# Optimization experiments

Hardware: AMD Instinct MI355X
Metric: run time of the kernel (lower is better)

## Reference

```python
import jax, jax.numpy as jnp
import numpy as np

D_MODEL = 256
N_FEATURES = 32768
N_BLOCKS = 8
MIN_FEATURES = 512
BATCH = 2048
ALPHA = 0.99          # RunningAvgNormalizer alpha
EPS_CTRL = 3e-4       # L1RegController eps
TARGET_L0 = 100.0


def _pareto_seg(n_features, n_blocks, min_features, rng):
    # mirrors get_pareto_block_bounds, returning per-feature block ids
    cdf = 1.0 - (np.arange(n_features - min_features + 1) / (n_features - min_features + 1)) ** 0.5
    pdf = np.concatenate([np.zeros(min_features), np.abs(cdf[1:] - cdf[:-1])])
    pdf = pdf / pdf.sum()
    sp = np.sort(rng.choice(n_features, size=n_blocks - 1, replace=False, p=pdf))
    return np.searchsorted(sp, np.arange(n_features), side='right').astype(np.int32)


def setup_inputs() -> dict:
    key = jax.random.key(0)
    k0, k1 = jax.random.split(key, 2)
    x = jax.random.normal(k0, (BATCH, D_MODEL), jnp.float32)
    W_enc = jax.random.normal(k1, (D_MODEL, N_FEATURES), jnp.float32) / np.sqrt(D_MODEL)
    b_enc = -0.04 * jnp.ones((N_FEATURES,), jnp.float32)
    W_dec = (0.1 * W_enc / jnp.linalg.norm(W_enc, axis=0, keepdims=True)).T
    b_dec = jnp.zeros((D_MODEL,), jnp.float32)
    bw = np.arange(1, N_BLOCKS + 1, dtype=np.float32) ** 1.0  # block_weight_power = 1.0
    block_weights = jnp.asarray(bw / bw.max())
    running_avg = jnp.asarray([np.sqrt(D_MODEL)], jnp.float32)  # warmed-up running norm
    l1_scale = jnp.ones((1,), jnp.float32)
    seg = jnp.asarray(_pareto_seg(N_FEATURES, N_BLOCKS, MIN_FEATURES, np.random.default_rng(0)))
    return {"x": x, "W_enc": W_enc, "b_enc": b_enc, "W_dec": W_dec, "b_dec": b_dec,
            "block_weights": block_weights, "running_avg": running_avg,
            "l1_scale": l1_scale, "seg": seg}


def reference(x, W_enc, b_enc, W_dec, b_dec, block_weights, running_avg, l1_scale, seg):
    K = block_weights.shape[0]
    B, d = x.shape
    # RunningAvgNormalizer.normalize(update=True): update EMA, then scale (no grad through EMA)
    ra = ALPHA * running_avg[0] + (1.0 - ALPHA) * jnp.mean(jnp.linalg.norm(x, axis=-1))
    ra = jax.lax.stop_gradient(ra)
    xn = x * (jnp.sqrt(jnp.float32(d)) / ra)
    acts = jax.nn.relu(xn @ W_enc + b_enc)                       # [B, F]
    Wd_norms = jnp.linalg.norm(W_dec, axis=1)                    # [F]
    # per-block log-loss: sum over block features of mean-over-batch log term
    per_feat = jnp.mean(jnp.log(acts * Wd_norms + 0.1) - jnp.log(0.1), axis=0)  # [F]
    block_l1 = jax.ops.segment_sum(per_feat, seg, num_segments=K)               # [K]
    l1_loss = jnp.mean(block_weights * jnp.cumsum(block_l1))
    # per-block decode: (acts masked to block) @ W_dec, sequential over K small blocks
    onehot = (seg[None, :] == jnp.arange(K)[:, None]).astype(acts.dtype)  # [K, F]
    block_preds = jax.lax.map(lambda m: (acts * m) @ W_dec, onehot)       # [K, B, d]
    cum_preds = jnp.cumsum(block_preds, axis=0) + b_dec                   # b_dec added to preds[0] pre-cumsum
    block_errs = jnp.mean(jnp.sum((cum_preds - xn[None]) ** 2, axis=-1), axis=-1) * block_weights
    mse_loss = jnp.mean(block_errs)
    # L1RegController (no-grad)
    avg_l0 = jax.lax.stop_gradient(jnp.sum(acts > 0).astype(jnp.float32) / B)
    l1_reg_scale = jnp.where(avg_l0 < TARGET_L0, l1_scale[0] * (1.0 - EPS_CTRL), l1_scale[0] * (1.0 + EPS_CTRL))
    loss = mse_loss + l1_reg_scale * l1_loss
    return loss
```

## Files before the change

### kernel.cpp

```cpp
#include <hip/hip_runtime.h>

typedef float  f32x4  __attribute__((ext_vector_type(4)));
typedef __bf16 bf16x8 __attribute__((ext_vector_type(8)));
typedef __bf16 bf16x4 __attribute__((ext_vector_type(4)));
typedef unsigned short u16;

#define BATCH 2048
#define DM    256
#define NFEAT 32768
#define NBLK  8
#define ALPHA_C   0.99f
#define EPS_CTRL  3e-4f
#define TARGET_L0 100.0f

#define BT    32
#define FC    2048
#define NCHUNK (NFEAT / FC)
#define MACRO 128
#define NMACRO (FC / MACRO)
#define NPMAX 24
#define ACTS_SZ (BT * MACRO)

#define WS_RA    0
#define WS_SCALE 1
#define WS_L0    2
#define WS_L1    4
#define WS_ERR   16
#define WSI_BND  32
#define WSI_PTN  40
#define WSI_PTS  41
#define WSI_PSEG 66
#define WS_WDN   256
#define PIECES_OFF_BYTES ((size_t)262144)
#define PIECES_BYTES ((size_t)NPMAX * BATCH * DM * 2)
#define WEP_OFF_BYTES (PIECES_OFF_BYTES + PIECES_BYTES)
#define WDP_OFF_BYTES (WEP_OFF_BYTES + (size_t)NFEAT * DM * 2)

#define RAW_BARRIER() asm volatile("s_waitcnt lgkmcnt(0)\n\ts_barrier" ::: "memory")

static __device__ inline u16 f2b(float f) {
    return __builtin_bit_cast(u16, (__bf16)f);
}
static __device__ inline float b2f(u16 u) {
    return (float)__builtin_bit_cast(__bf16, u);
}
static __device__ inline f32x4 mfma16(bf16x8 a, bf16x8 b, f32x4 c) {
    return __builtin_amdgcn_mfma_f32_16x16x32_bf16(a, b, c, 0, 0, 0);
}

__global__ __launch_bounds__(256) void k_prep(const float* __restrict__ x,
                                              const int* __restrict__ seg,
                                              float* ws) {
    const int bid = blockIdx.x;
    const int wave = threadIdx.x >> 6, lane = threadIdx.x & 63;
    if (bid < BATCH / 4) {
        const int row = bid * 4 + wave;
        const float4 v = *reinterpret_cast<const float4*>(x + (size_t)row * DM + lane * 4);
        float s = v.x * v.x + v.y * v.y + v.z * v.z + v.w * v.w;
        #pragma unroll
        for (int o = 32; o; o >>= 1) s += __shfl_xor(s, o);
        if (lane == 0) atomicAdd(&ws[WS_RA], sqrtf(s));
    } else {
        const int f = (bid - BATCH / 4) * 256 + threadIdx.x;
        if (f > 0 && f < NFEAT) {
            const int s = seg[f];
            if (s != seg[f - 1]) ((int*)ws)[WSI_BND + s] = f;
        }
    }
}

__global__ void k_pt2(const int* __restrict__ seg,
                      const float* __restrict__ ravg, float* ws) {
    __shared__ int stv[NCHUNK + NBLK];
    __shared__ int outL[NPMAX];
    __shared__ int NL;
    int* wsi = (int*)ws;
    const int t = threadIdx.x;
    if (t < NCHUNK) stv[t] = t * FC;
    else if (t < NCHUNK + NBLK - 1) stv[t] = wsi[WSI_BND + (t - NCHUNK + 1)];
    __syncthreads();
    if (t == 0) {
        int i = 0, j = NCHUNK, N = 0;
        while (i < NCHUNK || j < NCHUNK + NBLK - 1) {
            int v;
            if (i < NCHUNK && (j >= NCHUNK + NBLK - 1 || stv[i] <= stv[j])) v = stv[i++];
            else v = stv[j++];
            if (N == 0 || outL[N - 1] != v) outL[N++] = v;
        }
        NL = N;
    }
    __syncthreads();
    const int N = NL;
    if (t < N) {
        wsi[WSI_PTS + t] = outL[t];
        wsi[WSI_PSEG + t] = seg[outL[t]];
    }
    if (t == 0) {
        wsi[WSI_PTN] = N;
        wsi[WSI_PTS + N] = NFEAT;
        float ra = ALPHA_C * ravg[0] + (1.0f - ALPHA_C) * (ws[WS_RA] / (float)BATCH);
        ws[WS_SCALE] = 16.0f / ra;
    }
}

__global__ __launch_bounds__(256) void k_pack(const float* __restrict__ We,
                                              const float* __restrict__ Wd,
                                              u16* __restrict__ WeP,
                                              u16* __restrict__ WdP,
                                              float* ws) {
    __shared__ float tile[32][261];
    const int t = threadIdx.x;
    const int bid = blockIdx.x;
    if (bid < 1024) {
        const int kf = bid & 7, fblk = bid >> 3;
        const int f0 = fblk * 256;
        #pragma unroll
        for (int p = 0; p < 8; ++p) {
            const int r = p * 4 + (t >> 6);
            const int c = (t & 63) * 4;
            const float4 v = *reinterpret_cast<const float4*>(We + (size_t)(kf * 32 + r) * NFEAT + f0 + c);
            tile[r][c] = v.x; tile[r][c + 1] = v.y; tile[r][c + 2] = v.z; tile[r][c + 3] = v.w;
        }
        __syncthreads();
        #pragma unroll
        for (int p = 0; p < 4; ++p) {
            const int item = p * 256 + t;
            const int g = item >> 6, l = item & 63;
            const int F = fblk * 16 + g;
            bf16x8 v;
            #pragma unroll
            for (int i = 0; i < 8; ++i)
                v[i] = (__bf16)tile[(l >> 4) * 8 + i][g * 16 + (l & 15)];
            *reinterpret_cast<bf16x8*>(WeP + ((size_t)(F * 8 + kf) * 64 + l) * 8) = v;
        }
    } else {
        const int G = bid - 1024;
        #pragma unroll
        for (int p = 0; p < 8; ++p) {
            const int r = p * 4 + (t >> 6);
            const int c = (t & 63) * 4;
            const float4 v = *reinterpret_cast<const float4*>(Wd + (size_t)(G * 32 + r) * DM + c);
            tile[r][c] = v.x; tile[r][c + 1] = v.y; tile[r][c + 2] = v.z; tile[r][c + 3] = v.w;
        }
        __syncthreads();
        {
            const int row = t >> 3, part = t & 7;
            float s = 0.0f;
            #pragma unroll
            for (int j = 0; j < 32; ++j) {
                const float xv = tile[row][part * 32 + j];
                s += xv * xv;
            }
            s += __shfl_xor(s, 1); s += __shfl_xor(s, 2); s += __shfl_xor(s, 4);
            if (part == 0) ws[WS_WDN + G * 32 + row] = sqrtf(s);
        }
        #pragma unroll
        for (int p = 0; p < 4; ++p) {
            const int item = p * 256 + t;
            const int g = item >> 6, l = item & 63;
            bf16x8 v;
            #pragma unroll
            for (int i = 0; i < 8; ++i)
                v[i] = (__bf16)tile[(l >> 4) * 8 + i][g * 16 + (l & 15)];
            *reinterpret_cast<bf16x8*>(WdP + ((size_t)(g * 1024 + G) * 64 + l) * 8) = v;
        }
    }
}

__global__ __launch_bounds__(256, 2) void k_main(const float* __restrict__ x,
                                                 const float* __restrict__ be,
                                                 const int* __restrict__ seg,
                                                 float* __restrict__ ws,
                                                 u16* __restrict__ pieces,
                                                 const u16* __restrict__ WeP,
                                                 const u16* __restrict__ WdP) {
    __shared__ __align__(16) u16 xs[BT * DM];
    __shared__ __align__(16) u16 acts[2 * ACTS_SZ];
    __shared__ int segL[FC];
    __shared__ float lds_l1[NBLK];
    __shared__ unsigned lds_l0;
    __shared__ int s2s[NBLK];
    __shared__ int msegL[NMACRO];
    __shared__ int muniL[NMACRO];

    const int t = threadIdx.x;
    const int w = t >> 6;
    const int l = t & 63;
    const int l15 = l & 15, lg = l >> 4;
    const int f0 = blockIdx.x * FC;
    const int b0 = blockIdx.y * BT;
    const float scale = ws[WS_SCALE];
    const int* wsi = (const int*)ws;

    if (t < NBLK) lds_l1[t] = 0.0f;
    if (t == 0) lds_l0 = 0u;
    if (t < NPMAX) {
        const int N = wsi[WSI_PTN];
        if (t < N) {
            const int ps = wsi[WSI_PTS + t];
            if (ps >= f0 && ps < f0 + FC) s2s[wsi[WSI_PSEG + t]] = t;
        }
    }

    #pragma unroll
    for (int p = 0; p < 2; ++p)
        reinterpret_cast<int4*>(segL)[t + p * 256] =
            reinterpret_cast<const int4*>(seg + f0)[t + p * 256];

    #pragma unroll
    for (int p = 0; p < 8; ++p) {
        const int row = p * 4 + (t >> 6);
        const int col = (t & 63) * 4;
        const float4 v = *reinterpret_cast<const float4*>(x + (size_t)(b0 + row) * DM + col);
        bf16x4 h;
        h[0] = (__bf16)(v.x * scale); h[1] = (__bf16)(v.y * scale);
        h[2] = (__bf16)(v.z * scale); h[3] = (__bf16)(v.w * scale);
        const int e = (((row >> 4) * 8 + (col >> 5)) * 512 + ((col >> 3) & 3) * 128 + (row & 15) * 8 + (col & 7));
        *reinterpret_cast<bf16x4*>(&xs[e]) = h;
    }
    __syncthreads();
    if (t < NMACRO) {
        msegL[t] = segL[t * MACRO];
        muniL[t] = (segL[t * MACRO] == segL[t * MACRO + MACRO - 1]);
    }
    __syncthreads();

    f32x4 pacc[2][4];
    #pragma unroll
    for (int i = 0; i < 2; ++i)
        #pragma unroll
        for (int j = 0; j < 4; ++j) pacc[i][j] = (f32x4)0.0f;

    int cur = msegL[0];
    float l1a0 = 0.0f, l1a1 = 0.0f;
    int myseg = -1;
    unsigned l0c = 0u;
    const int Dg0 = 4 * w;

    auto flush = [&](int s) {
        u16* pb = pieces + (size_t)s2s[s] * (BATCH * DM);
        #pragma unroll
        for (int rt = 0; rt < 2; ++rt)
            #pragma unroll
            for (int ct = 0; ct < 4; ++ct)
                #pragma unroll
                for (int r = 0; r < 4; ++r) {
                    const int row = b0 + 16 * rt + lg * 4 + r;
                    const int col = 64 * w + 16 * ct + l15;
                    pb[(size_t)row * DM + col] = f2b(pacc[rt][ct][r]);
                    pacc[rt][ct][r] = 0.0f;
                }
    };

    auto encodeR = [&](f32x4 (&eacc)[2][2], bf16x8 (&we)[2][8]) {
        #pragma unroll
        for (int kf = 0; kf < 8; ++kf) {
            bf16x8 a[2];
            #pragma unroll
            for (int rt = 0; rt < 2; ++rt)
                a[rt] = *reinterpret_cast<const bf16x8*>(&xs[((rt * 8 + kf) * 64 + l) * 8]);
            #pragma unroll
            for (int rt = 0; rt < 2; ++rt)
                #pragma unroll
                for (int ct = 0; ct < 2; ++ct)
                    eacc[rt][ct] = mfma16(a[rt], we[ct][kf], eacc[rt][ct]);
        }
    };

    auto epilogue = [&](int it, f32x4 (&eacc)[2][2], const float* biasv, const float* wdnv) {
        const bool uni = (muniL[it] != 0);
        u16* ab = acts + (it & 1) * ACTS_SZ;
        const int fbl = it * MACRO;
        #pragma unroll
        for (int ct = 0; ct < 2; ++ct) {
            const int s = uni ? msegL[it] : segL[fbl + 32 * w + 16 * ct + l15];
            if (s != myseg) {
                if (myseg >= 0) atomicAdd(&lds_l1[myseg], l1a0 + l1a1);
                l1a0 = 0.0f; l1a1 = 0.0f; myseg = s;
            }
            #pragma unroll
            for (int rt = 0; rt < 2; ++rt)
                #pragma unroll
                for (int r = 0; r < 4; ++r) {
                    float a = eacc[rt][ct][r] + biasv[ct];
                    a = fmaxf(a, 0.0f);
                    l0c += (unsigned)__popcll(__ballot(a > 0.0f));
                    if (rt == 0) l1a0 += __logf(fmaf(a, wdnv[ct], 1.0f));
                    else         l1a1 += __logf(fmaf(a, wdnv[ct], 1.0f));
                    const int e = (rt * 4 + w) * 512 + (2 * ct + (l15 >> 3)) * 128 + (lg * 4 + r) * 8 + (l15 & 7);
                    ab[e] = f2b(a);
                }
        }
    };

    auto decodeR = [&](int ms, bf16x8 (&wdv)[4][4]) {
        const u16* ab = acts + (ms & 1) * ACTS_SZ;
        if (muniL[ms]) {
            const int s = msegL[ms];
            if (s != cur) { flush(cur); cur = s; }
            #pragma unroll
            for (int kf = 0; kf < 4; ++kf) {
                bf16x8 a[2];
                #pragma unroll
                for (int rt = 0; rt < 2; ++rt)
                    a[rt] = *reinterpret_cast<const bf16x8*>(&ab[((rt * 4 + kf) * 64 + l) * 8]);
                #pragma unroll
                for (int rt = 0; rt < 2; ++rt)
                    #pragma unroll
                    for (int ct = 0; ct < 4; ++ct)
                        pacc[rt][ct] = mfma16(a[rt], wdv[ct][kf], pacc[rt][ct]);
            }
        } else {
            const int fbl = ms * MACRO;
            #pragma unroll
            for (int kf = 0; kf < 4; ++kf) {
                const int W0 = fbl + kf * 32;
                const int s0 = segL[W0], s1 = segL[W0 + 31];
                if (s0 == s1) {
                    if (s0 != cur) { flush(cur); cur = s0; }
                    bf16x8 a[2];
                    #pragma unroll
                    for (int rt = 0; rt < 2; ++rt)
                        a[rt] = *reinterpret_cast<const bf16x8*>(&ab[((rt * 4 + kf) * 64 + l) * 8]);
                    #pragma unroll
                    for (int rt = 0; rt < 2; ++rt)
                        #pragma unroll
                        for (int ct = 0; ct < 4; ++ct)
                            pacc[rt][ct] = mfma16(a[rt], wdv[ct][kf], pacc[rt][ct]);
                } else {
                    int lo = 0;
                    while (lo < 32) {
                        const int s = segL[W0 + lo];
                        int hi = lo + 1;
                        while (hi < 32 && segL[W0 + hi] == s) ++hi;
                        if (s != cur) { flush(cur); cur = s; }
                        bf16x8 a[2];
                        #pragma unroll
                        for (int rt = 0; rt < 2; ++rt) {
                            a[rt] = *reinterpret_cast<const bf16x8*>(&ab[((rt * 4 + kf) * 64 + l) * 8]);
                            #pragma unroll
                            for (int i = 0; i < 8; ++i) {
                                const int kl = lg * 8 + i;
                                if (kl < lo || kl >= hi) a[rt][i] = (__bf16)0.0f;
                            }
                        }
                        #pragma unroll
                        for (int rt = 0; rt < 2; ++rt)
                            #pragma unroll
                            for (int ct = 0; ct < 4; ++ct)
                                pacc[rt][ct] = mfma16(a[rt], wdv[ct][kf], pacc[rt][ct]);
                        lo = hi;
                    }
                }
            }
        }
    };

    {
        bf16x8 we[2][8];
        const int F0 = (f0 >> 4) + 2 * w;
        #pragma unroll
        for (int kf = 0; kf < 8; ++kf)
            #pragma unroll
            for (int ct = 0; ct < 2; ++ct)
                we[ct][kf] = *reinterpret_cast<const bf16x8*>(WeP + (((size_t)(F0 + ct) * 8 + kf) * 64 + l) * 8);
        float biasv[2], wdnv[2];
        #pragma unroll
        for (int ct = 0; ct < 2; ++ct) {
            const int fg = f0 + 32 * w + 16 * ct + l15;
            biasv[ct] = be[fg];
            wdnv[ct] = ws[WS_WDN + fg] * 10.0f;
        }
        f32x4 eacc[2][2];
        #pragma unroll
        for (int i = 0; i < 2; ++i)
            #pragma unroll
            for (int j = 0; j < 2; ++j) eacc[i][j] = (f32x4)0.0f;
        encodeR(eacc, we);
        epilogue(0, eacc, biasv, wdnv);
    }

    for (int it = 1; it <= NMACRO; ++it) {
        RAW_BARRIER();
        const int itm1 = it - 1;

        if (it < NMACRO) {
            bf16x8 we[2][8];
            const int F0 = ((f0 + it * MACRO) >> 4) + 2 * w;
            #pragma unroll
            for (int kf = 0; kf < 8; ++kf)
                #pragma unroll
                for (int ct = 0; ct < 2; ++ct)
                    we[ct][kf] = *reinterpret_cast<const bf16x8*>(WeP + (((size_t)(F0 + ct) * 8 + kf) * 64 + l) * 8);
            bf16x8 wdv[4][4];
            const int G0 = (f0 + itm1 * MACRO) >> 5;
            #pragma unroll
            for (int kf = 0; kf < 4; ++kf)
                #pragma unroll
                for (int ct = 0; ct < 4; ++ct)
                    wdv[ct][kf] = *reinterpret_cast<const bf16x8*>(WdP + (((size_t)(Dg0 + ct) * 1024 + G0 + kf) * 64 + l) * 8);
            float biasv[2], wdnv[2];
            #pragma unroll
            for (int ct = 0; ct < 2; ++ct) {
                const int fg = f0 + it * MACRO + 32 * w + 16 * ct + l15;
                biasv[ct] = be[fg];
                wdnv[ct] = ws[WS_WDN + fg] * 10.0f;
            }

            f32x4 eacc[2][2];
            #pragma unroll
            for (int i = 0; i < 2; ++i)
                #pragma unroll
                for (int j = 0; j < 2; ++j) eacc[i][j] = (f32x4)0.0f;
            encodeR(eacc, we);
            decodeR(itm1, wdv);
            epilogue(it, eacc, biasv, wdnv);
        } else {
            bf16x8 wdv[4][4];
            const int G0 = (f0 + itm1 * MACRO) >> 5;
            #pragma unroll
            for (int kf = 0; kf < 4; ++kf)
                #pragma unroll
                for (int ct = 0; ct < 4; ++ct)
                    wdv[ct][kf] = *reinterpret_cast<const bf16x8*>(WdP + (((size_t)(Dg0 + ct) * 1024 + G0 + kf) * 64 + l) * 8);
            decodeR(itm1, wdv);
        }
    }

    flush(cur);
    if (myseg >= 0) atomicAdd(&lds_l1[myseg], l1a0 + l1a1);
    if (l == 0) atomicAdd(&lds_l0, l0c);
    __syncthreads();
    if (t < NBLK) atomicAdd(&ws[WS_L1 + t], lds_l1[t]);
    if (t == 0) atomicAdd(((unsigned*)ws) + WS_L0, lds_l0);
}


__global__ __launch_bounds__(256) void k_err(const float* __restrict__ x,
                                             const float* __restrict__ bd,
                                             float* ws,
                                             const u16* __restrict__ pieces) {
    const int b = blockIdx.x, t = threadIdx.x;
    const int wave = t >> 6, lane = t & 63;
    const int* wsi = (const int*)ws;
    const int N = wsi[WSI_PTN];
    const float scale = ws[WS_SCALE];
    const float xv = x[(size_t)b * DM + t] * scale;
    float p = bd[t];
    __shared__ float lds[NBLK][4];
    for (int i = 0; i < N; ++i) {
        p += b2f(pieces[(size_t)i * (BATCH * DM) + (size_t)b * DM + t]);
        const int sg = wsi[WSI_PSEG + i];
        const bool end = (i == N - 1) || (wsi[WSI_PSEG + i + 1] != sg);
        if (end) {
            const float d = p - xv;
            float e = d * d;
            #pragma unroll
            for (int o = 32; o; o >>= 1) e += __shfl_xor(e, o);
            if (lane == 0) lds[sg][wave] = e;
        }
    }
    __syncthreads();
    if (t < NBLK) {
        const float s = lds[t][0] + lds[t][1] + lds[t][2] + lds[t][3];
        atomicAdd(&ws[WS_ERR + t], s);
    }
}

__global__ void k_loss(const float* __restrict__ bw,
                       const float* __restrict__ l1s,
                       const float* ws, float* out) {
    float cum = 0.0f, l1 = 0.0f, mse = 0.0f;
    for (int k = 0; k < NBLK; ++k) {
        cum += ws[WS_L1 + k] / (float)BATCH;
        l1 += bw[k] * cum;
        mse += bw[k] * (ws[WS_ERR + k] / (float)BATCH);
    }
    l1 *= (1.0f / NBLK);
    mse *= (1.0f / NBLK);
    const unsigned l0 = ((const unsigned*)ws)[WS_L0];
    const float avg_l0 = (float)l0 / (float)BATCH;
    const float rs = l1s[0] * (avg_l0 < TARGET_L0 ? (1.0f - EPS_CTRL) : (1.0f + EPS_CTRL));
    out[0] = mse + rs * l1;
}


extern "C" void kernel_launch(void* const* d_in, const int* in_sizes, int n_in,
                              void* d_out, int out_size, void* d_ws, size_t ws_size,
                              hipStream_t stream) {
    const float* x    = (const float*)d_in[0];
    const float* We   = (const float*)d_in[1];
    const float* be   = (const float*)d_in[2];
    const float* Wd   = (const float*)d_in[3];
    const float* bd   = (const float*)d_in[4];
    const float* bw   = (const float*)d_in[5];
    const float* ravg = (const float*)d_in[6];
    const float* l1s  = (const float*)d_in[7];
    const int*   seg  = (const int*)d_in[8];
    float* out = (float*)d_out;
    float* ws  = (float*)d_ws;
    u16* pieces = (u16*)((char*)d_ws + PIECES_OFF_BYTES);
    u16* WeP = (u16*)((char*)d_ws + WEP_OFF_BYTES);
    u16* WdP = (u16*)((char*)d_ws + WDP_OFF_BYTES);

    hipMemsetAsync(d_ws, 0, 1024, stream);
    k_prep<<<BATCH / 4 + NFEAT / 256, 256, 0, stream>>>(x, seg, ws);
    k_pack<<<2048, 256, 0, stream>>>(We, Wd, WeP, WdP, ws);
    k_pt2<<<1, 64, 0, stream>>>(seg, ravg, ws);
    dim3 g(NFEAT / FC, BATCH / BT);
    k_main<<<g, 256, 0, stream>>>(x, be, seg, ws, pieces, WeP, WdP);
    k_err<<<BATCH, 256, 0, stream>>>(x, bd, ws, pieces);
    k_loss<<<1, 1, 0, stream>>>(bw, l1s, ws, out);
}
```

Before: 230.5 us.

## Double batch tile to 64 rows with 8 waves per block in k_main

Doubles the k_main batch tile from 32 to 64 rows and the block size from 256 to 512 threads. Waves are arranged as 2 row groups by 4 column groups, so each wave pair shares the same encoder and decoder weight fragments across twice as many batch rows. This halves how often packed weights are reloaded per batch row, at the cost of more LDS for activations and inputs, higher register pressure under the 512-thread launch bound, and half as many blocks in the grid.

```diff
diff --git a/kernel.cpp b/kernel.cpp
--- a/kernel.cpp
+++ b/kernel.cpp
@@ -13,7 +13,7 @@
 #define EPS_CTRL  3e-4f
 #define TARGET_L0 100.0f
 
-#define BT    32
+#define BT    64
 #define FC    2048
 #define NCHUNK (NFEAT / FC)
 #define MACRO 128
@@ -167,7 +167,7 @@
     }
 }
 
-__global__ __launch_bounds__(256, 2) void k_main(const float* __restrict__ x,
+__global__ __launch_bounds__(512, 2) void k_main(const float* __restrict__ x,
                                                  const float* __restrict__ be,
                                                  const int* __restrict__ seg,
                                                  float* __restrict__ ws,
@@ -185,6 +185,8 @@
 
     const int t = threadIdx.x;
     const int w = t >> 6;
+    const int wr = w >> 2;
+    const int wc = w & 3;
     const int l = t & 63;
     const int l15 = l & 15, lg = l >> 4;
     const int f0 = blockIdx.x * FC;
@@ -202,14 +204,11 @@
         }
     }
 
-    #pragma unroll
-    for (int p = 0; p < 2; ++p)
-        reinterpret_cast<int4*>(segL)[t + p * 256] =
-            reinterpret_cast<const int4*>(seg + f0)[t + p * 256];
+    reinterpret_cast<int4*>(segL)[t] = reinterpret_cast<const int4*>(seg + f0)[t];
 
     #pragma unroll
     for (int p = 0; p < 8; ++p) {
-        const int row = p * 4 + (t >> 6);
+        const int row = p * 8 + (t >> 6);
         const int col = (t & 63) * 4;
         const float4 v = *reinterpret_cast<const float4*>(x + (size_t)(b0 + row) * DM + col);
         bf16x4 h;
@@ -235,7 +234,7 @@
     float l1a0 = 0.0f, l1a1 = 0.0f;
     int myseg = -1;
     unsigned l0c = 0u;
-    const int Dg0 = 4 * w;
+    const int Dg0 = 4 * wc;
 
     auto flush = [&](int s) {
         u16* pb = pieces + (size_t)s2s[s] * (BATCH * DM);
@@ -245,8 +244,8 @@
             for (int ct = 0; ct < 4; ++ct)
                 #pragma unroll
                 for (int r = 0; r < 4; ++r) {
-                    const int row = b0 + 16 * rt + lg * 4 + r;
-                    const int col = 64 * w + 16 * ct + l15;
+                    const int row = b0 + 32 * wr + 16 * rt + lg * 4 + r;
+                    const int col = 64 * wc + 16 * ct + l15;
                     pb[(size_t)row * DM + col] = f2b(pacc[rt][ct][r]);
                     pacc[rt][ct][r] = 0.0f;
                 }
@@ -258,7 +257,7 @@
             bf16x8 a[2];
             #pragma unroll
             for (int rt = 0; rt < 2; ++rt)
-                a[rt] = *reinterpret_cast<const bf16x8*>(&xs[((rt * 8 + kf) * 64 + l) * 8]);
+                a[rt] = *reinterpret_cast<const bf16x8*>(&xs[(((wr * 2 + rt) * 8 + kf) * 64 + l) * 8]);
             #pragma unroll
             for (int rt = 0; rt < 2; ++rt)
                 #pragma unroll
@@ -273,7 +272,7 @@
         const int fbl = it * MACRO;
         #pragma unroll
         for (int ct = 0; ct < 2; ++ct) {
-            const int s = uni ? msegL[it] : segL[fbl + 32 * w + 16 * ct + l15];
+            const int s = uni ? msegL[it] : segL[fbl + 32 * wc + 16 * ct + l15];
             if (s != myseg) {
                 if (myseg >= 0) atomicAdd(&lds_l1[myseg], l1a0 + l1a1);
                 l1a0 = 0.0f; l1a1 = 0.0f; myseg = s;
@@ -287,7 +286,7 @@
                     l0c += (unsigned)__popcll(__ballot(a > 0.0f));
                     if (rt == 0) l1a0 += __logf(fmaf(a, wdnv[ct], 1.0f));
                     else         l1a1 += __logf(fmaf(a, wdnv[ct], 1.0f));
-                    const int e = (rt * 4 + w) * 512 + (2 * ct + (l15 >> 3)) * 128 + (lg * 4 + r) * 8 + (l15 & 7);
+                    const int e = ((wr * 2 + rt) * 4 + wc) * 512 + (2 * ct + (l15 >> 3)) * 128 + (lg * 4 + r) * 8 + (l15 & 7);
                     ab[e] = f2b(a);
                 }
         }
@@ -303,7 +302,7 @@
                 bf16x8 a[2];
                 #pragma unroll
                 for (int rt = 0; rt < 2; ++rt)
-                    a[rt] = *reinterpret_cast<const bf16x8*>(&ab[((rt * 4 + kf) * 64 + l) * 8]);
+                    a[rt] = *reinterpret_cast<const bf16x8*>(&ab[(((wr * 2 + rt) * 4 + kf) * 64 + l) * 8]);
                 #pragma unroll
                 for (int rt = 0; rt < 2; ++rt)
                     #pragma unroll
@@ -321,7 +320,7 @@
                     bf16x8 a[2];
                     #pragma unroll
                     for (int rt = 0; rt < 2; ++rt)
-                        a[rt] = *reinterpret_cast<const bf16x8*>(&ab[((rt * 4 + kf) * 64 + l) * 8]);
+                        a[rt] = *reinterpret_cast<const bf16x8*>(&ab[(((wr * 2 + rt) * 4 + kf) * 64 + l) * 8]);
                     #pragma unroll
                     for (int rt = 0; rt < 2; ++rt)
                         #pragma unroll
@@ -337,7 +336,7 @@
                         bf16x8 a[2];
                         #pragma unroll
                         for (int rt = 0; rt < 2; ++rt) {
-                            a[rt] = *reinterpret_cast<const bf16x8*>(&ab[((rt * 4 + kf) * 64 + l) * 8]);
+                            a[rt] = *reinterpret_cast<const bf16x8*>(&ab[(((wr * 2 + rt) * 4 + kf) * 64 + l) * 8]);
                             #pragma unroll
                             for (int i = 0; i < 8; ++i) {
                                 const int kl = lg * 8 + i;
@@ -358,7 +357,7 @@
 
     {
         bf16x8 we[2][8];
-        const int F0 = (f0 >> 4) + 2 * w;
+        const int F0 = (f0 >> 4) + 2 * wc;
         #pragma unroll
         for (int kf = 0; kf < 8; ++kf)
             #pragma unroll
@@ -367,7 +366,7 @@
         float biasv[2], wdnv[2];
         #pragma unroll
         for (int ct = 0; ct < 2; ++ct) {
-            const int fg = f0 + 32 * w + 16 * ct + l15;
+            const int fg = f0 + 32 * wc + 16 * ct + l15;
             biasv[ct] = be[fg];
             wdnv[ct] = ws[WS_WDN + fg] * 10.0f;
         }
@@ -386,7 +385,7 @@
 
         if (it < NMACRO) {
             bf16x8 we[2][8];
-            const int F0 = ((f0 + it * MACRO) >> 4) + 2 * w;
+            const int F0 = ((f0 + it * MACRO) >> 4) + 2 * wc;
             #pragma unroll
             for (int kf = 0; kf < 8; ++kf)
                 #pragma unroll
@@ -402,7 +401,7 @@
             float biasv[2], wdnv[2];
             #pragma unroll
             for (int ct = 0; ct < 2; ++ct) {
-                const int fg = f0 + it * MACRO + 32 * w + 16 * ct + l15;
+                const int fg = f0 + it * MACRO + 32 * wc + 16 * ct + l15;
                 biasv[ct] = be[fg];
                 wdnv[ct] = ws[WS_WDN + fg] * 10.0f;
             }
@@ -508,7 +507,7 @@
     k_pack<<<2048, 256, 0, stream>>>(We, Wd, WeP, WdP, ws);
     k_pt2<<<1, 64, 0, stream>>>(seg, ravg, ws);
     dim3 g(NFEAT / FC, BATCH / BT);
-    k_main<<<g, 256, 0, stream>>>(x, be, seg, ws, pieces, WeP, WdP);
+    k_main<<<g, 512, 0, stream>>>(x, be, seg, ws, pieces, WeP, WdP);
     k_err<<<BATCH, 256, 0, stream>>>(x, bd, ws, pieces);
     k_loss<<<1, 1, 0, stream>>>(bw, l1s, ws, out);
 }
```

After: 251.6 us. 9.2% more time.

## Switch encoder and decoder GEMMs from bf16 to fp8 MFMA with scaled weights

Applied to the files above, without the earlier changes.

Packs W_enc and W_dec into fp8 e4m3 with fixed power-of-two scales, stores normalized inputs and activations in LDS as fp8, and uses the fp8 16x16x32 MFMA in both the encode and decode loops, undoing the scales afterward. The goal is to halve weight and LDS traffic and use the higher fp8 matrix throughput. Partial-segment masking now uses a byte mask instead of per-element zeroing. The cost is a large loss of precision in activations and weights, which may push the loss outside tolerance. The fp8 MFMA also uses the same 16x16x32 shape, so per-instruction throughput may not improve.

```diff
diff --git a/kernel.cpp b/kernel.cpp
--- a/kernel.cpp
+++ b/kernel.cpp
@@ -1,9 +1,10 @@
 #include <hip/hip_runtime.h>
+#include <hip/hip_fp8.h>
 
 typedef float  f32x4  __attribute__((ext_vector_type(4)));
-typedef __bf16 bf16x8 __attribute__((ext_vector_type(8)));
-typedef __bf16 bf16x4 __attribute__((ext_vector_type(4)));
 typedef unsigned short u16;
+typedef unsigned int   u32;
+typedef unsigned long long u64;
 
 #define BATCH 2048
 #define DM    256
@@ -20,6 +21,11 @@
 #define NMACRO (FC / MACRO)
 #define NPMAX 24
 #define ACTS_SZ (BT * MACRO)
+
+#define SCL_WE 8.0f
+#define INV_WE 0.125f
+#define SCL_WD 16.0f
+#define INV_WD 0.0625f
 
 #define WS_RA    0
 #define WS_SCALE 1
@@ -34,7 +40,7 @@
 #define PIECES_OFF_BYTES ((size_t)262144)
 #define PIECES_BYTES ((size_t)NPMAX * BATCH * DM * 2)
 #define WEP_OFF_BYTES (PIECES_OFF_BYTES + PIECES_BYTES)
-#define WDP_OFF_BYTES (WEP_OFF_BYTES + (size_t)NFEAT * DM * 2)
+#define WDP_OFF_BYTES (WEP_OFF_BYTES + (size_t)NFEAT * DM)
 
 #define RAW_BARRIER() asm volatile("s_waitcnt lgkmcnt(0)\n\ts_barrier" ::: "memory")
 
@@ -44,8 +50,17 @@
 static __device__ inline float b2f(u16 u) {
     return (float)__builtin_bit_cast(__bf16, u);
 }
-static __device__ inline f32x4 mfma16(bf16x8 a, bf16x8 b, f32x4 c) {
-    return __builtin_amdgcn_mfma_f32_16x16x32_bf16(a, b, c, 0, 0, 0);
+static __device__ inline u32 f2f8x2(float a, float b) {
+#if __has_builtin(__builtin_amdgcn_cvt_pk_fp8_f32)
+    return ((u32)__builtin_amdgcn_cvt_pk_fp8_f32(a, b, 0, false)) & 0xFFFFu;
+#else
+    __hip_fp8_e4m3 ha(a), hb(b);
+    return (u32)(*reinterpret_cast<unsigned char*>(&ha)) |
+           ((u32)(*reinterpret_cast<unsigned char*>(&hb)) << 8);
+#endif
+}
+static __device__ inline f32x4 mfma8(u64 a, u64 b, f32x4 c) {
+    return __builtin_amdgcn_mfma_f32_16x16x32_fp8_fp8((long)a, (long)b, c, 0, 0, 0);
 }
 
 __global__ __launch_bounds__(256) void k_prep(const float* __restrict__ x,
@@ -105,8 +120,8 @@
 
 __global__ __launch_bounds__(256) void k_pack(const float* __restrict__ We,
                                               const float* __restrict__ Wd,
-                                              u16* __restrict__ WeP,
-                                              u16* __restrict__ WdP,
+                                              unsigned char* __restrict__ WeP,
+                                              unsigned char* __restrict__ WdP,
                                               float* ws) {
     __shared__ float tile[32][261];
     const int t = threadIdx.x;
@@ -127,11 +142,13 @@
             const int item = p * 256 + t;
             const int g = item >> 6, l = item & 63;
             const int F = fblk * 16 + g;
-            bf16x8 v;
+            float tv[8];
             #pragma unroll
             for (int i = 0; i < 8; ++i)
-                v[i] = (__bf16)tile[(l >> 4) * 8 + i][g * 16 + (l & 15)];
-            *reinterpret_cast<bf16x8*>(WeP + ((size_t)(F * 8 + kf) * 64 + l) * 8) = v;
+                tv[i] = tile[(l >> 4) * 8 + i][g * 16 + (l & 15)] * SCL_WE;
+            const u32 lo = f2f8x2(tv[0], tv[1]) | (f2f8x2(tv[2], tv[3]) << 16);
+            const u32 hi = f2f8x2(tv[4], tv[5]) | (f2f8x2(tv[6], tv[7]) << 16);
+            *reinterpret_cast<u64*>(WeP + ((size_t)(F * 8 + kf) * 64 + l) * 8) = (u64)lo | ((u64)hi << 32);
         }
     } else {
         const int G = bid - 1024;
@@ -158,11 +175,13 @@
         for (int p = 0; p < 4; ++p) {
             const int item = p * 256 + t;
             const int g = item >> 6, l = item & 63;
-            bf16x8 v;
+            float tv[8];
             #pragma unroll
             for (int i = 0; i < 8; ++i)
-                v[i] = (__bf16)tile[(l >> 4) * 8 + i][g * 16 + (l & 15)];
-            *reinterpret_cast<bf16x8*>(WdP + ((size_t)(g * 1024 + G) * 64 + l) * 8) = v;
+                tv[i] = tile[(l >> 4) * 8 + i][g * 16 + (l & 15)] * SCL_WD;
+            const u32 lo = f2f8x2(tv[0], tv[1]) | (f2f8x2(tv[2], tv[3]) << 16);
+            const u32 hi = f2f8x2(tv[4], tv[5]) | (f2f8x2(tv[6], tv[7]) << 16);
+            *reinterpret_cast<u64*>(WdP + ((size_t)(g * 1024 + G) * 64 + l) * 8) = (u64)lo | ((u64)hi << 32);
         }
     }
 }
@@ -172,10 +191,10 @@
                                                  const int* __restrict__ seg,
                                                  float* __restrict__ ws,
                                                  u16* __restrict__ pieces,
-                                                 const u16* __restrict__ WeP,
-                                                 const u16* __restrict__ WdP) {
-    __shared__ __align__(16) u16 xs[BT * DM];
-    __shared__ __align__(16) u16 acts[2 * ACTS_SZ];
+                                                 const unsigned char* __restrict__ WeP,
+                                                 const unsigned char* __restrict__ WdP) {
+    __shared__ __align__(16) unsigned char xs[BT * DM];
+    __shared__ __align__(16) unsigned char acts[2 * ACTS_SZ];
     __shared__ int segL[FC];
     __shared__ float lds_l1[NBLK];
     __shared__ unsigned lds_l0;
@@ -212,11 +231,10 @@
         const int row = p * 4 + (t >> 6);
         const int col = (t & 63) * 4;
         const float4 v = *reinterpret_cast<const float4*>(x + (size_t)(b0 + row) * DM + col);
-        bf16x4 h;
-        h[0] = (__bf16)(v.x * scale); h[1] = (__bf16)(v.y * scale);
-        h[2] = (__bf16)(v.z * scale); h[3] = (__bf16)(v.w * scale);
+        const u32 w01 = f2f8x2(v.x * scale, v.y * scale);
+        const u32 w23 = f2f8x2(v.z * scale, v.w * scale);
         const int e = (((row >> 4) * 8 + (col >> 5)) * 512 + ((col >> 3) & 3) * 128 + (row & 15) * 8 + (col & 7));
-        *reinterpret_cast<bf16x4*>(&xs[e]) = h;
+        *reinterpret_cast<u32*>(&xs[e]) = w01 | (w23 << 16);
     }
     __syncthreads();
     if (t < NMACRO) {
@@ -247,29 +265,29 @@
                 for (int r = 0; r < 4; ++r) {
                     const int row = b0 + 16 * rt + lg * 4 + r;
                     const int col = 64 * w + 16 * ct + l15;
-                    pb[(size_t)row * DM + col] = f2b(pacc[rt][ct][r]);
+                    pb[(size_t)row * DM + col] = f2b(pacc[rt][ct][r] * INV_WD);
                     pacc[rt][ct][r] = 0.0f;
                 }
     };
 
-    auto encodeR = [&](f32x4 (&eacc)[2][2], bf16x8 (&we)[2][8]) {
+    auto encodeR = [&](f32x4 (&eacc)[2][2], u64 (&we)[2][8]) {
         #pragma unroll
         for (int kf = 0; kf < 8; ++kf) {
-            bf16x8 a[2];
+            u64 a[2];
             #pragma unroll
             for (int rt = 0; rt < 2; ++rt)
-                a[rt] = *reinterpret_cast<const bf16x8*>(&xs[((rt * 8 + kf) * 64 + l) * 8]);
+                a[rt] = *reinterpret_cast<const u64*>(&xs[((rt * 8 + kf) * 64 + l) * 8]);
             #pragma unroll
             for (int rt = 0; rt < 2; ++rt)
                 #pragma unroll
                 for (int ct = 0; ct < 2; ++ct)
-                    eacc[rt][ct] = mfma16(a[rt], we[ct][kf], eacc[rt][ct]);
+                    eacc[rt][ct] = mfma8(a[rt], we[ct][kf], eacc[rt][ct]);
         }
     };
 
     auto epilogue = [&](int it, f32x4 (&eacc)[2][2], const float* biasv, const float* wdnv) {
         const bool uni = (muniL[it] != 0);
-        u16* ab = acts + (it & 1) * ACTS_SZ;
+        unsigned char* ab = acts + (it & 1) * ACTS_SZ;
         const int fbl = it * MACRO;
         #pragma unroll
         for (int ct = 0; ct < 2; ++ct) {
@@ -279,36 +297,44 @@
                 l1a0 = 0.0f; l1a1 = 0.0f; myseg = s;
             }
             #pragma unroll
-            for (int rt = 0; rt < 2; ++rt)
+            for (int rt = 0; rt < 2; ++rt) {
+                float av[4];
                 #pragma unroll
                 for (int r = 0; r < 4; ++r) {
-                    float a = eacc[rt][ct][r] + biasv[ct];
+                    float a = fmaf(eacc[rt][ct][r], INV_WE, biasv[ct]);
                     a = fmaxf(a, 0.0f);
                     l0c += (unsigned)__popcll(__ballot(a > 0.0f));
                     if (rt == 0) l1a0 += __logf(fmaf(a, wdnv[ct], 1.0f));
                     else         l1a1 += __logf(fmaf(a, wdnv[ct], 1.0f));
-                    const int e = (rt * 4 + w) * 512 + (2 * ct + (l15 >> 3)) * 128 + (lg * 4 + r) * 8 + (l15 & 7);
-                    ab[e] = f2b(a);
+                    av[r] = a;
                 }
+                const u32 p01 = f2f8x2(av[0], av[1]);
+                const u32 p23 = f2f8x2(av[2], av[3]);
+                const int e0 = (rt * 4 + w) * 512 + (2 * ct + (l15 >> 3)) * 128 + (lg * 4) * 8 + (l15 & 7);
+                ab[e0]      = (unsigned char)(p01 & 0xFF);
+                ab[e0 + 8]  = (unsigned char)((p01 >> 8) & 0xFF);
+                ab[e0 + 16] = (unsigned char)(p23 & 0xFF);
+                ab[e0 + 24] = (unsigned char)((p23 >> 8) & 0xFF);
+            }
         }
     };
 
-    auto decodeR = [&](int ms, bf16x8 (&wdv)[4][4]) {
-        const u16* ab = acts + (ms & 1) * ACTS_SZ;
+    auto decodeR = [&](int ms, u64 (&wdv)[4][4]) {
+        const unsigned char* ab = acts + (ms & 1) * ACTS_SZ;
         if (muniL[ms]) {
             const int s = msegL[ms];
             if (s != cur) { flush(cur); cur = s; }
             #pragma unroll
             for (int kf = 0; kf < 4; ++kf) {
-                bf16x8 a[2];
+                u64 a[2];
                 #pragma unroll
                 for (int rt = 0; rt < 2; ++rt)
-                    a[rt] = *reinterpret_cast<const bf16x8*>(&ab[((rt * 4 + kf) * 64 + l) * 8]);
+                    a[rt] = *reinterpret_cast<const u64*>(&ab[((rt * 4 + kf) * 64 + l) * 8]);
                 #pragma unroll
                 for (int rt = 0; rt < 2; ++rt)
                     #pragma unroll
                     for (int ct = 0; ct < 4; ++ct)
-                        pacc[rt][ct] = mfma16(a[rt], wdv[ct][kf], pacc[rt][ct]);
+                        pacc[rt][ct] = mfma8(a[rt], wdv[ct][kf], pacc[rt][ct]);
             }
         } else {
             const int fbl = ms * MACRO;
@@ -318,15 +344,15 @@
                 const int s0 = segL[W0], s1 = segL[W0 + 31];
                 if (s0 == s1) {
                     if (s0 != cur) { flush(cur); cur = s0; }
-                    bf16x8 a[2];
+                    u64 a[2];
                     #pragma unroll
                     for (int rt = 0; rt < 2; ++rt)
-                        a[rt] = *reinterpret_cast<const bf16x8*>(&ab[((rt * 4 + kf) * 64 + l) * 8]);
+                        a[rt] = *reinterpret_cast<const u64*>(&ab[((rt * 4 + kf) * 64 + l) * 8]);
                     #pragma unroll
                     for (int rt = 0; rt < 2; ++rt)
                         #pragma unroll
                         for (int ct = 0; ct < 4; ++ct)
-                            pacc[rt][ct] = mfma16(a[rt], wdv[ct][kf], pacc[rt][ct]);
+                            pacc[rt][ct] = mfma8(a[rt], wdv[ct][kf], pacc[rt][ct]);
                 } else {
                     int lo = 0;
                     while (lo < 32) {
@@ -334,21 +360,19 @@
                         int hi = lo + 1;
                         while (hi < 32 && segL[W0 + hi] == s) ++hi;
                         if (s != cur) { flush(cur); cur = s; }
-                        bf16x8 a[2];
+                        const int loB = min(max(lo - lg * 8, 0), 8);
+                        const int hiB = min(max(hi - lg * 8, 0), 8);
+                        const int n = hiB - loB;
+                        u64 mask = 0;
+                        if (n >= 8) mask = ~0ull;
+                        else if (n > 0) mask = ((1ull << (n * 8)) - 1ull) << (loB * 8);
                         #pragma unroll
                         for (int rt = 0; rt < 2; ++rt) {
-                            a[rt] = *reinterpret_cast<const bf16x8*>(&ab[((rt * 4 + kf) * 64 + l) * 8]);
-                            #pragma unroll
-                            for (int i = 0; i < 8; ++i) {
-                                const int kl = lg * 8 + i;
-                                if (kl < lo || kl >= hi) a[rt][i] = (__bf16)0.0f;
-                            }
-                        }
-                        #pragma unroll
-                        for (int rt = 0; rt < 2; ++rt)
+                            const u64 a = (*reinterpret_cast<const u64*>(&ab[((rt * 4 + kf) * 64 + l) * 8])) & mask;
                             #pragma unroll
                             for (int ct = 0; ct < 4; ++ct)
-                                pacc[rt][ct] = mfma16(a[rt], wdv[ct][kf], pacc[rt][ct]);
+                                pacc[rt][ct] = mfma8(a, wdv[ct][kf], pacc[rt][ct]);
+                        }
                         lo = hi;
                     }
                 }
@@ -357,13 +381,13 @@
     };
 
     {
-        bf16x8 we[2][8];
+        u64 we[2][8];
         const int F0 = (f0 >> 4) + 2 * w;
         #pragma unroll
         for (int kf = 0; kf < 8; ++kf)
             #pragma unroll
             for (int ct = 0; ct < 2; ++ct)
-                we[ct][kf] = *reinterpret_cast<const bf16x8*>(WeP + (((size_t)(F0 + ct) * 8 + kf) * 64 + l) * 8);
+                we[ct][kf] = *reinterpret_cast<const u64*>(WeP + (((size_t)(F0 + ct) * 8 + kf) * 64 + l) * 8);
         float biasv[2], wdnv[2];
         #pragma unroll
         for (int ct = 0; ct < 2; ++ct) {
@@ -385,20 +409,20 @@
         const int itm1 = it - 1;
 
         if (it < NMACRO) {
-            bf16x8 we[2][8];
+            u64 we[2][8];
             const int F0 = ((f0 + it * MACRO) >> 4) + 2 * w;
             #pragma unroll
             for (int kf = 0; kf < 8; ++kf)
                 #pragma unroll
                 for (int ct = 0; ct < 2; ++ct)
-                    we[ct][kf] = *reinterpret_cast<const bf16x8*>(WeP + (((size_t)(F0 + ct) * 8 + kf) * 64 + l) * 8);
-            bf16x8 wdv[4][4];
+                    we[ct][kf] = *reinterpret_cast<const u64*>(WeP + (((size_t)(F0 + ct) * 8 + kf) * 64 + l) * 8);
+            u64 wdv[4][4];
             const int G0 = (f0 + itm1 * MACRO) >> 5;
             #pragma unroll
             for (int kf = 0; kf < 4; ++kf)
                 #pragma unroll
                 for (int ct = 0; ct < 4; ++ct)
-                    wdv[ct][kf] = *reinterpret_cast<const bf16x8*>(WdP + (((size_t)(Dg0 + ct) * 1024 + G0 + kf) * 64 + l) * 8);
+                    wdv[ct][kf] = *reinterpret_cast<const u64*>(WdP + (((size_t)(Dg0 + ct) * 1024 + G0 + kf) * 64 + l) * 8);
             float biasv[2], wdnv[2];
             #pragma unroll
             for (int ct = 0; ct < 2; ++ct) {
@@ -416,13 +440,13 @@
             decodeR(itm1, wdv);
             epilogue(it, eacc, biasv, wdnv);
         } else {
-            bf16x8 wdv[4][4];
+            u64 wdv[4][4];
             const int G0 = (f0 + itm1 * MACRO) >> 5;
             #pragma unroll
             for (int kf = 0; kf < 4; ++kf)
                 #pragma unroll
                 for (int ct = 0; ct < 4; ++ct)
-                    wdv[ct][kf] = *reinterpret_cast<const bf16x8*>(WdP + (((size_t)(Dg0 + ct) * 1024 + G0 + kf) * 64 + l) * 8);
+                    wdv[ct][kf] = *reinterpret_cast<const u64*>(WdP + (((size_t)(Dg0 + ct) * 1024 + G0 + kf) * 64 + l) * 8);
             decodeR(itm1, wdv);
         }
     }
@@ -500,8 +524,8 @@
     float* out = (float*)d_out;
     float* ws  = (float*)d_ws;
     u16* pieces = (u16*)((char*)d_ws + PIECES_OFF_BYTES);
-    u16* WeP = (u16*)((char*)d_ws + WEP_OFF_BYTES);
-    u16* WdP = (u16*)((char*)d_ws + WDP_OFF_BYTES);
+    unsigned char* WeP = (unsigned char*)d_ws + WEP_OFF_BYTES;
+    unsigned char* WdP = (unsigned char*)d_ws + WDP_OFF_BYTES;
 
     hipMemsetAsync(d_ws, 0, 1024, stream);
     k_prep<<<BATCH / 4 + NFEAT / 256, 256, 0, stream>>>(x, seg, ws);
```

Measured after the change: 212.1 us (median of 2 runs). -8.0%, faster.
